# Kernel optimization log

Measured on AMD Instinct MI355X. Metric: run time of the kernel, lower is better.

Reference implementation:

```python
import jax, jax.numpy as jnp
import numpy as np

N_NODES = 30000
N_EDGES = 480000
IN_CH, NF, OUT_CH = 64, 128, 3
N_HIDDEN = 6  # GCN(num_layers=7): conv0 (in->nf) + 6 convs (nf->nf)
SLOPE = 0.02


def setup_inputs() -> dict:
    key = jax.random.key(0)
    ks = jax.random.split(key, 8)
    x = jax.random.normal(ks[0], (N_NODES, IN_CH), dtype=jnp.float32)
    edge_index = jax.random.randint(ks[1], (2, N_EDGES), 0, N_NODES, dtype=jnp.int64)
    W0 = jax.random.normal(ks[2], (IN_CH, NF), dtype=jnp.float32) * (1.0 / np.sqrt(IN_CH))
    b0 = jnp.zeros((NF,), dtype=jnp.float32)
    Wh = jax.random.normal(ks[3], (N_HIDDEN, NF, NF), dtype=jnp.float32) * (1.0 / np.sqrt(NF))
    bh = jnp.zeros((N_HIDDEN, NF), dtype=jnp.float32)
    Wout = jax.random.normal(ks[4], (NF, OUT_CH), dtype=jnp.float32) * (1.0 / np.sqrt(NF))
    bout = jnp.zeros((OUT_CH,), dtype=jnp.float32)
    return {"x": x, "edge_index": edge_index, "W0": W0, "b0": b0,
            "Wh": Wh, "bh": bh, "Wout": Wout, "bout": bout}


def _gcn_norm(edge_index, n):
    # PyG GCNConv default: add self-loops, symmetric normalization D^-1/2 (A+I) D^-1/2
    loop = jnp.arange(n, dtype=edge_index.dtype)
    src = jnp.concatenate([edge_index[0], loop])
    dst = jnp.concatenate([edge_index[1], loop])
    deg = jax.ops.segment_sum(jnp.ones_like(dst, dtype=jnp.float32), dst, num_segments=n)
    dinv = jax.lax.rsqrt(deg)  # deg >= 1 due to self-loops
    norm = dinv[src] * dinv[dst]  # [E+N]
    return src, dst, norm


def _gcn_conv(h, W, b, src, dst, norm, n):
    h = h @ W                                   # [N, F_out]
    msg = h[src] * norm[:, None]                # gather + scale  [E+N, F_out]
    out = jax.ops.segment_sum(msg, dst, num_segments=n)  # scatter-add
    return out + b


def reference(x, edge_index, W0, b0, Wh, bh, Wout, bout):
    n = x.shape[0]
    src, dst, norm = _gcn_norm(edge_index, n)
    # 7-layer GCN stack with LeakyReLU(0.02) between layers; dropout is
    # identity in eval mode (training=False).
    h = _gcn_conv(x, W0, b0, src, dst, norm, n)
    for i in range(N_HIDDEN):
        h = jax.nn.leaky_relu(h, SLOPE)
        h = _gcn_conv(h, Wh[i], bh[i], src, dst, norm, n)
    # outer forward: leaky_relu -> dropout(eval=identity) -> out conv -> tanh*0.5
    h = jax.nn.leaky_relu(h, SLOPE)
    h = _gcn_conv(h, Wout, bout, src, dst, norm, n)
    return jnp.tanh(h) * 0.5
```

## Files before the change

kernel.cpp:

```cpp
#include <hip/hip_runtime.h>
#include <hip/hip_fp16.h>
#include <math.h>

#define NN 30000
#define NE 480000
#define NB 118
#define INVSCALE (1.0f / 4096.0f)

typedef _Float16 half8 __attribute__((ext_vector_type(8)));
typedef float floatx4 __attribute__((ext_vector_type(4)));
typedef float floatx2 __attribute__((ext_vector_type(2)));

__device__ __forceinline__ float lrelu(float v) { return v > 0.0f ? v : v * 0.02f; }

__device__ __forceinline__ float4 fma4(float4 v, float w, float4 a) {
    a.x = fmaf(v.x, w, a.x);
    a.y = fmaf(v.y, w, a.y);
    a.z = fmaf(v.z, w, a.z);
    a.w = fmaf(v.w, w, a.w);
    return a;
}

__device__ __forceinline__ float4 loadh4(const __half* p) {
    uint2 raw = *(const uint2*)p;
    float2 f0 = __half22float2(*(__half2*)&raw.x);
    float2 f1 = __half22float2(*(__half2*)&raw.y);
    return make_float4(f0.x, f0.y, f1.x, f1.y);
}

__device__ __forceinline__ void loadf8x8(const unsigned char* p, float4* lo, float4* hi) {
    uint2 raw = *(const uint2*)p;
    floatx2 a = __builtin_amdgcn_cvt_pk_f32_fp8(raw.x, false);
    floatx2 b = __builtin_amdgcn_cvt_pk_f32_fp8(raw.x, true);
    floatx2 c = __builtin_amdgcn_cvt_pk_f32_fp8(raw.y, false);
    floatx2 d = __builtin_amdgcn_cvt_pk_f32_fp8(raw.y, true);
    *lo = make_float4(a.x, a.y, b.x, b.y);
    *hi = make_float4(c.x, c.y, d.x, d.y);
}

__device__ __forceinline__ void stnt_f8(unsigned char* p, float v) {
    int pk = __builtin_amdgcn_cvt_pk_fp8_f32(v, v, 0, false);
    __builtin_nontemporal_store((unsigned char)pk, p);
}


__global__ void k_count(const int* __restrict__ ei, int* __restrict__ cnt,
                        const float* __restrict__ W0, const float* __restrict__ Wh,
                        const float* __restrict__ b0, const float* __restrict__ bh,
                        const float* __restrict__ x,
                        __half* __restrict__ W0t, __half* __restrict__ Wht,
                        float* __restrict__ bs, __half* __restrict__ x16) {
    int g = blockIdx.x * 256 + threadIdx.x;
    if (g < NE) atomicAdd(&cnt[ei[NE + g]], 1);
    {
        float4 v = *(const float4*)&x[(size_t)g * 4];
        __half2 a = __floats2half2_rn(v.x, v.y);
        __half2 b = __floats2half2_rn(v.z, v.w);
        uint2 pk;
        pk.x = *(unsigned int*)&a;
        pk.y = *(unsigned int*)&b;
        *(uint2*)&x16[(size_t)g * 4] = pk;
    }
    if (g < 8192) {
        int k = g >> 7, n = g & 127;
        W0t[n * 64 + k] = __float2half(W0[g] * 64.0f);
    } else if (g < 8192 + 98304) {
        int j = g - 8192;
        int l = j >> 14;
        int r = j & 16383;
        int k = r >> 7, n = r & 127;
        Wht[l * 16384 + n * 128 + k] = __float2half(Wh[j] * 2.0f);
    } else if (g < 8192 + 98304 + 896) {
        int j = g - 8192 - 98304;
        float sc;
        if (j < 128) sc = 64.0f;
        else sc = (float)(1 << (7 + ((j - 128) >> 7)));
        bs[j] = (j < 128 ? b0[j] : bh[j - 128]) * sc;
    }
}

__global__ void k_scan1(const int* __restrict__ cnt, int* __restrict__ bsum,
                        float* __restrict__ dinv) {
    __shared__ int sd[256];
    int tid = threadIdx.x;
    int i = blockIdx.x * 256 + tid;
    int v = (i < NN) ? cnt[i] : 0;
    if (i < NN) dinv[i] = 1.0f / sqrtf((float)(v + 1));
    sd[tid] = v;
    __syncthreads();
    for (int off = 128; off > 0; off >>= 1) {
        if (tid < off) sd[tid] += sd[tid + off];
        __syncthreads();
    }
    if (tid == 0) bsum[blockIdx.x] = sd[0];
}

__global__ void k_scan3(const int* __restrict__ cnt, const int* __restrict__ bsum,
                        int* __restrict__ row_ptr, int* __restrict__ cursor) {
    __shared__ int sd[256];
    __shared__ int offs[128];
    int tid = threadIdx.x;
    if (tid < 128) offs[tid] = (tid < blockIdx.x) ? bsum[tid] : 0;
    __syncthreads();
    for (int o = 64; o > 0; o >>= 1) {
        if (tid < o) offs[tid] += offs[tid + o];
        __syncthreads();
    }
    int i = blockIdx.x * 256 + tid;
    int v = (i < NN) ? cnt[i] : 0;
    sd[tid] = v;
    __syncthreads();
    for (int off = 1; off < 256; off <<= 1) {
        int t = (tid >= off) ? sd[tid - off] : 0;
        __syncthreads();
        sd[tid] += t;
        __syncthreads();
    }
    if (i < NN) {
        int excl = offs[0] + sd[tid] - v;
        row_ptr[i] = excl;
        cursor[i] = excl;
        if (i == NN - 1) row_ptr[NN] = excl + v;
    }
}

__global__ void k_fill(const int* __restrict__ ei, const float* __restrict__ dinv,
                       int* __restrict__ cursor, int2* __restrict__ csr) {
    int e = blockIdx.x * 256 + threadIdx.x;
    if (e < NE) {
        int s = ei[e];
        int d = ei[NE + e];
        int pos = atomicAdd(&cursor[d], 1);
        float w = dinv[s] * dinv[d];
        csr[pos] = make_int2(s, __float_as_int(w));
    }
}


__launch_bounds__(256)
__global__ void k_layer0(const __half* __restrict__ x, const int* __restrict__ row_ptr,
                         const int2* __restrict__ csr, const float* __restrict__ dinv,
                         const __half* __restrict__ Wt, const float* __restrict__ bias,
                         unsigned char* __restrict__ out8) {
    __shared__ _Float16 hsF[2 * 4 * 16 * 8];
    int tid = threadIdx.x;
    int node0 = blockIdx.x * 16;
    {
        int nl = tid >> 4;
        int node = node0 + nl;
        int c = (tid & 15) * 4;
        float di = dinv[node];
        float w0 = di * di;
        float4 hv = loadh4(&x[(size_t)node * 64 + c]);
        float4 acc[8];
        acc[0] = make_float4(hv.x * w0, hv.y * w0, hv.z * w0, hv.w * w0);
        #pragma unroll
        for (int j = 1; j < 8; j++) acc[j] = make_float4(0.f, 0.f, 0.f, 0.f);
        int e = row_ptr[node];
        int e1 = row_ptr[node + 1];
        for (; e + 8 <= e1; e += 8) {
            int2 sw[8];
            #pragma unroll
            for (int j = 0; j < 8; j++) sw[j] = csr[e + j];
            float4 v[8];
            #pragma unroll
            for (int j = 0; j < 8; j++) v[j] = loadh4(&x[(size_t)sw[j].x * 64 + c]);
            #pragma unroll
            for (int j = 0; j < 8; j++) acc[j] = fma4(v[j], __int_as_float(sw[j].y), acc[j]);
        }
        for (; e < e1; ++e) {
            int2 sw = csr[e];
            float4 v = loadh4(&x[(size_t)sw.x * 64 + c]);
            acc[0] = fma4(v, __int_as_float(sw.y), acc[0]);
        }
        #pragma unroll
        for (int j = 1; j < 8; j++) {
            acc[0].x += acc[j].x;
            acc[0].y += acc[j].y;
            acc[0].z += acc[j].z;
            acc[0].w += acc[j].w;
        }
        int ks = c >> 5, quad = (c >> 3) & 3, jj = c & 7;
        __half2 p0 = __floats2half2_rn(acc[0].x, acc[0].y);
        __half2 p1 = __floats2half2_rn(acc[0].z, acc[0].w);
        uint2 pk;
        pk.x = *(unsigned int*)&p0;
        pk.y = *(unsigned int*)&p1;
        *(uint2*)&hsF[((ks * 4 + quad) * 16 + nl) * 8 + jj] = pk;
    }
    __syncthreads();
    int wave = tid >> 6, lane = tid & 63, quad = lane >> 4, ln = lane & 15;
    half8 afrag[2];
    #pragma unroll
    for (int ks = 0; ks < 2; ks++)
        afrag[ks] = *(const half8*)&hsF[((ks * 4 + quad) * 16 + ln) * 8];
    #pragma unroll
    for (int tc = 0; tc < 2; tc++) {
        int tt = wave + tc * 4;
        floatx4 acc = (floatx4){0.f, 0.f, 0.f, 0.f};
        #pragma unroll
        for (int ks = 0; ks < 2; ks++) {
            half8 b = *(const half8*)&Wt[(size_t)(tt * 16 + ln) * 64 + ks * 32 + quad * 8];
            acc = __builtin_amdgcn_mfma_f32_16x16x32_f16(afrag[ks], b, acc, 0, 0, 0);
        }
        int col = tt * 16 + ln;
        float bb = bias[col];
        #pragma unroll
        for (int r = 0; r < 4; r++) {
            int row = node0 + quad * 4 + r;
            stnt_f8(&out8[(size_t)row * 128 + col], lrelu(acc[r] + bb));
        }
    }
}

template <bool LAST>
__launch_bounds__(256)
__global__ void k_layer_h(const unsigned char* __restrict__ h, const int* __restrict__ row_ptr,
                          const int2* __restrict__ csr, const float* __restrict__ dinv,
                          const __half* __restrict__ Wt, const float* __restrict__ bias,
                          unsigned char* __restrict__ out8, const float* __restrict__ Wout,
                          float* __restrict__ u) {
    __shared__ _Float16 hsF[4 * 4 * 16 * 8];
    __shared__ float uacc[4][16][3];
    int tid = threadIdx.x;
    int node0 = blockIdx.x * 16;
    {
        int nl = tid >> 4;
        int node = node0 + nl;
        int c = (tid & 15) * 8;
        float di = dinv[node];
        float w0 = di * di;
        float4 hlo, hhi;
        loadf8x8(&h[(size_t)node * 128 + c], &hlo, &hhi);
        float4 acc[4][2];
        acc[0][0] = make_float4(hlo.x * w0, hlo.y * w0, hlo.z * w0, hlo.w * w0);
        acc[0][1] = make_float4(hhi.x * w0, hhi.y * w0, hhi.z * w0, hhi.w * w0);
        #pragma unroll
        for (int j = 1; j < 4; j++) {
            acc[j][0] = make_float4(0.f, 0.f, 0.f, 0.f);
            acc[j][1] = make_float4(0.f, 0.f, 0.f, 0.f);
        }
        int e = row_ptr[node];
        int e1 = row_ptr[node + 1];
        for (; e + 4 <= e1; e += 4) {
            int2 sw[4];
            #pragma unroll
            for (int j = 0; j < 4; j++) sw[j] = csr[e + j];
            float4 vlo[4], vhi[4];
            #pragma unroll
            for (int j = 0; j < 4; j++)
                loadf8x8(&h[(size_t)sw[j].x * 128 + c], &vlo[j], &vhi[j]);
            #pragma unroll
            for (int j = 0; j < 4; j++) {
                float w = __int_as_float(sw[j].y);
                acc[j][0] = fma4(vlo[j], w, acc[j][0]);
                acc[j][1] = fma4(vhi[j], w, acc[j][1]);
            }
        }
        for (; e < e1; ++e) {
            int2 sw = csr[e];
            float4 vlo, vhi;
            loadf8x8(&h[(size_t)sw.x * 128 + c], &vlo, &vhi);
            float w = __int_as_float(sw.y);
            acc[0][0] = fma4(vlo, w, acc[0][0]);
            acc[0][1] = fma4(vhi, w, acc[0][1]);
        }
        #pragma unroll
        for (int j = 1; j < 4; j++) {
            acc[0][0].x += acc[j][0].x; acc[0][0].y += acc[j][0].y;
            acc[0][0].z += acc[j][0].z; acc[0][0].w += acc[j][0].w;
            acc[0][1].x += acc[j][1].x; acc[0][1].y += acc[j][1].y;
            acc[0][1].z += acc[j][1].z; acc[0][1].w += acc[j][1].w;
        }
        int ks = c >> 5, quad = (c >> 3) & 3;
        __half2 p0 = __floats2half2_rn(acc[0][0].x, acc[0][0].y);
        __half2 p1 = __floats2half2_rn(acc[0][0].z, acc[0][0].w);
        __half2 p2 = __floats2half2_rn(acc[0][1].x, acc[0][1].y);
        __half2 p3 = __floats2half2_rn(acc[0][1].z, acc[0][1].w);
        uint4 pk;
        pk.x = *(unsigned int*)&p0;
        pk.y = *(unsigned int*)&p1;
        pk.z = *(unsigned int*)&p2;
        pk.w = *(unsigned int*)&p3;
        *(uint4*)&hsF[((ks * 4 + quad) * 16 + nl) * 8] = pk;
    }
    __syncthreads();
    int wave = tid >> 6, lane = tid & 63, quad = lane >> 4, ln = lane & 15;
    half8 afrag[4];
    #pragma unroll
    for (int ks = 0; ks < 4; ks++)
        afrag[ks] = *(const half8*)&hsF[((ks * 4 + quad) * 16 + ln) * 8];

    float up[4][3];
    if (LAST) {
        #pragma unroll
        for (int r = 0; r < 4; r++)
            #pragma unroll
            for (int cc = 0; cc < 3; cc++) up[r][cc] = 0.f;
    }

    #pragma unroll
    for (int tc = 0; tc < 2; tc++) {
        int tt = wave + tc * 4;
        floatx4 acc = (floatx4){0.f, 0.f, 0.f, 0.f};
        #pragma unroll
        for (int ks = 0; ks < 4; ks++) {
            half8 b = *(const half8*)&Wt[(size_t)(tt * 16 + ln) * 128 + ks * 32 + quad * 8];
            acc = __builtin_amdgcn_mfma_f32_16x16x32_f16(afrag[ks], b, acc, 0, 0, 0);
        }
        int col = tt * 16 + ln;
        float bb = bias[col];
        if (LAST) {
            float w0o = Wout[col * 3 + 0];
            float w1o = Wout[col * 3 + 1];
            float w2o = Wout[col * 3 + 2];
            #pragma unroll
            for (int r = 0; r < 4; r++) {
                float hv = lrelu(acc[r] + bb);
                up[r][0] = fmaf(hv, w0o, up[r][0]);
                up[r][1] = fmaf(hv, w1o, up[r][1]);
                up[r][2] = fmaf(hv, w2o, up[r][2]);
            }
        } else {
            #pragma unroll
            for (int r = 0; r < 4; r++) {
                int row = node0 + quad * 4 + r;
                stnt_f8(&out8[(size_t)row * 128 + col], lrelu(acc[r] + bb));
            }
        }
    }

    if (LAST) {
        #pragma unroll
        for (int m = 1; m < 16; m <<= 1) {
            #pragma unroll
            for (int r = 0; r < 4; r++) {
                #pragma unroll
                for (int cc = 0; cc < 3; cc++)
                    up[r][cc] += __shfl_xor(up[r][cc], m);
            }
        }
        if (ln == 0) {
            #pragma unroll
            for (int r = 0; r < 4; r++) {
                #pragma unroll
                for (int cc = 0; cc < 3; cc++)
                    uacc[wave][quad * 4 + r][cc] = up[r][cc];
            }
        }
        __syncthreads();
        if (tid < 48) {
            int row = tid / 3, cc = tid % 3;
            float s = (uacc[0][row][cc] + uacc[1][row][cc]) +
                      (uacc[2][row][cc] + uacc[3][row][cc]);
            u[(size_t)(node0 + row) * 3 + cc] = s;
        }
    }
}


__global__ void k_agg_out(const float* __restrict__ u, const int* __restrict__ row_ptr,
                          const int2* __restrict__ csr, const float* __restrict__ dinv,
                          const float* __restrict__ bout, float* __restrict__ out) {
    int node = blockIdx.x * 256 + threadIdx.x;
    if (node >= NN) return;
    float di = dinv[node], w0 = di * di;
    float s0 = u[(size_t)node * 3 + 0] * w0;
    float s1 = u[(size_t)node * 3 + 1] * w0;
    float s2 = u[(size_t)node * 3 + 2] * w0;
    float b0a = 0.f, b1a = 0.f, b2a = 0.f;
    int e = row_ptr[node];
    int e1 = row_ptr[node + 1];
    for (; e + 2 <= e1; e += 2) {
        int2 swa = csr[e], swb = csr[e + 1];
        float wa = __int_as_float(swa.y), wb = __int_as_float(swb.y);
        const float* ua = &u[(size_t)swa.x * 3];
        const float* ub = &u[(size_t)swb.x * 3];
        s0 = fmaf(ua[0], wa, s0);
        s1 = fmaf(ua[1], wa, s1);
        s2 = fmaf(ua[2], wa, s2);
        b0a = fmaf(ub[0], wb, b0a);
        b1a = fmaf(ub[1], wb, b1a);
        b2a = fmaf(ub[2], wb, b2a);
    }
    for (; e < e1; ++e) {
        int2 sw = csr[e];
        float w = __int_as_float(sw.y);
        const float* us = &u[(size_t)sw.x * 3];
        s0 = fmaf(us[0], w, s0);
        s1 = fmaf(us[1], w, s1);
        s2 = fmaf(us[2], w, s2);
    }
    out[(size_t)node * 3 + 0] = tanhf((s0 + b0a) * INVSCALE + bout[0]) * 0.5f;
    out[(size_t)node * 3 + 1] = tanhf((s1 + b1a) * INVSCALE + bout[1]) * 0.5f;
    out[(size_t)node * 3 + 2] = tanhf((s2 + b2a) * INVSCALE + bout[2]) * 0.5f;
}


extern "C" void kernel_launch(void* const* d_in, const int* in_sizes, int n_in,
                              void* d_out, int out_size, void* d_ws, size_t ws_size,
                              hipStream_t stream) {
    const float* x        = (const float*)d_in[0];
    const int*   ei       = (const int*)d_in[1];
    const float* W0       = (const float*)d_in[2];
    const float* b0       = (const float*)d_in[3];
    const float* Wh       = (const float*)d_in[4];
    const float* bh       = (const float*)d_in[5];
    const float* Wout     = (const float*)d_in[6];
    const float* bout     = (const float*)d_in[7];
    float* out            = (float*)d_out;

    char* ws = (char*)d_ws;
    float*  bufA   = (float*)(ws + 0);
    unsigned char* bufB8 = (unsigned char*)(ws + 15360000);
    unsigned char* bufC8 = (unsigned char*)(ws + 23040000);
    __half* x16    = (__half*)(ws + 30720000);
    __half* W0t16  = (__half*)(ws + 34560000);
    __half* Wht16  = (__half*)(ws + 34576384);
    float*  bs     = (float*)(ws + 34772992);
    float*  dinv   = (float*)(ws + 34776576);
    int*    cnt    = (int*)  (ws + 34896576);
    int*    row_ptr= (int*)  (ws + 35016576);
    int*    cursor = (int*)  (ws + 35136640);
    int2*   csr    = (int2*) (ws + 35256640);

    int* bsum = (int*)bufA;

    hipMemsetAsync(cnt, 0, NN * sizeof(int), stream);
    k_count<<<(NE + 255) / 256, 256, 0, stream>>>(ei, cnt, W0, Wh, b0, bh, x,
                                                  W0t16, Wht16, bs, x16);
    k_scan1<<<NB, 256, 0, stream>>>(cnt, bsum, dinv);
    k_scan3<<<NB, 256, 0, stream>>>(cnt, bsum, row_ptr, cursor);
    k_fill<<<(NE + 255) / 256, 256, 0, stream>>>(ei, dinv, cursor, csr);

    k_layer0<<<NN / 16, 256, 0, stream>>>(x16, row_ptr, csr, dinv, W0t16, bs, bufB8);

    unsigned char* hin = bufB8;
    unsigned char* hout = bufC8;
    for (int i = 0; i < 5; i++) {
        k_layer_h<false><<<NN / 16, 256, 0, stream>>>(hin, row_ptr, csr, dinv,
                                                      Wht16 + (size_t)i * 16384,
                                                      bs + 128 + (size_t)i * 128, hout,
                                                      Wout, bufA);
        unsigned char* t = hin; hin = hout; hout = t;
    }
    k_layer_h<true><<<NN / 16, 256, 0, stream>>>(hin, row_ptr, csr, dinv,
                                                 Wht16 + (size_t)5 * 16384,
                                                 bs + 128 + (size_t)5 * 128, hout,
                                                 Wout, bufA );

    k_agg_out<<<(NN + 255) / 256, 256, 0, stream>>>(bufA, row_ptr, csr, dinv, bout, out);
}
```

Measured before the change: 297.5 us.

## Split each node's edge gather across two half-waves and merge scans into one kernel

Layer kernels now use 512 threads per 16-node tile. Each node's neighbor list is split between two 16-lane groups that each handle 8 edges per iteration, with clamped tail loads and a shuffle reduction at the end. The MFMA stage then uses 8 waves, one output column tile each, instead of 4 waves doing two tiles each. This aims to raise memory-level parallelism for the irregular gathers, but adds predicated loads, a cross-lane reduction and more registers per block. The two-kernel prefix scan is replaced by a single 1024-thread block scan, which saves a launch but serializes the work onto one CU.

```diff
diff --git a/kernel.cpp b/kernel.cpp
--- a/kernel.cpp
+++ b/kernel.cpp
@@ -4,8 +4,9 @@
 
 #define NN 30000
 #define NE 480000
-#define NB 118
+#define NTILE 1875
 #define INVSCALE (1.0f / 4096.0f)
+
 
 typedef _Float16 half8 __attribute__((ext_vector_type(8)));
 typedef float floatx4 __attribute__((ext_vector_type(4)));
@@ -21,15 +22,13 @@
     return a;
 }
 
-__device__ __forceinline__ float4 loadh4(const __half* p) {
-    uint2 raw = *(const uint2*)p;
+__device__ __forceinline__ float4 cvth4(uint2 raw) {
     float2 f0 = __half22float2(*(__half2*)&raw.x);
     float2 f1 = __half22float2(*(__half2*)&raw.y);
     return make_float4(f0.x, f0.y, f1.x, f1.y);
 }
 
-__device__ __forceinline__ void loadf8x8(const unsigned char* p, float4* lo, float4* hi) {
-    uint2 raw = *(const uint2*)p;
+__device__ __forceinline__ void cvtf8x8(uint2 raw, float4* lo, float4* hi) {
     floatx2 a = __builtin_amdgcn_cvt_pk_f32_fp8(raw.x, false);
     floatx2 b = __builtin_amdgcn_cvt_pk_f32_fp8(raw.x, true);
     floatx2 c = __builtin_amdgcn_cvt_pk_f32_fp8(raw.y, false);
@@ -41,6 +40,14 @@
 __device__ __forceinline__ void stnt_f8(unsigned char* p, float v) {
     int pk = __builtin_amdgcn_cvt_pk_fp8_f32(v, v, 0, false);
     __builtin_nontemporal_store((unsigned char)pk, p);
+}
+
+__device__ __forceinline__ float4 xadd16(float4 a) {
+    a.x += __shfl_xor(a.x, 16);
+    a.y += __shfl_xor(a.y, 16);
+    a.z += __shfl_xor(a.z, 16);
+    a.w += __shfl_xor(a.w, 16);
+    return a;
 }
 
 
@@ -79,49 +86,52 @@
     }
 }
 
-__global__ void k_scan1(const int* __restrict__ cnt, int* __restrict__ bsum,
-                        float* __restrict__ dinv) {
-    __shared__ int sd[256];
+__global__ void k_scan(const int* __restrict__ cnt, int* __restrict__ row_ptr,
+                       int* __restrict__ cursor, float* __restrict__ dinv) {
+    __shared__ int part[1024];
     int tid = threadIdx.x;
-    int i = blockIdx.x * 256 + tid;
-    int v = (i < NN) ? cnt[i] : 0;
-    if (i < NN) dinv[i] = 1.0f / sqrtf((float)(v + 1));
-    sd[tid] = v;
+    const int CH = 32;
+    int base = tid * CH;
+    int s = 0;
+    #pragma unroll
+    for (int i = 0; i < CH; i += 4) {
+        int idx = base + i;
+        if (idx < NN) {
+            int4 v = *(const int4*)&cnt[idx];
+            s += v.x + v.y + v.z + v.w;
+        }
+    }
+    part[tid] = s;
     __syncthreads();
-    for (int off = 128; off > 0; off >>= 1) {
-        if (tid < off) sd[tid] += sd[tid + off];
+    for (int off = 1; off < 1024; off <<= 1) {
+        int t = (tid >= off) ? part[tid - off] : 0;
         __syncthreads();
-    }
-    if (tid == 0) bsum[blockIdx.x] = sd[0];
-}
-
-__global__ void k_scan3(const int* __restrict__ cnt, const int* __restrict__ bsum,
-                        int* __restrict__ row_ptr, int* __restrict__ cursor) {
-    __shared__ int sd[256];
-    __shared__ int offs[128];
-    int tid = threadIdx.x;
-    if (tid < 128) offs[tid] = (tid < blockIdx.x) ? bsum[tid] : 0;
-    __syncthreads();
-    for (int o = 64; o > 0; o >>= 1) {
-        if (tid < o) offs[tid] += offs[tid + o];
+        part[tid] += t;
         __syncthreads();
     }
-    int i = blockIdx.x * 256 + tid;
-    int v = (i < NN) ? cnt[i] : 0;
-    sd[tid] = v;
-    __syncthreads();
-    for (int off = 1; off < 256; off <<= 1) {
-        int t = (tid >= off) ? sd[tid - off] : 0;
-        __syncthreads();
-        sd[tid] += t;
-        __syncthreads();
-    }
-    if (i < NN) {
-        int excl = offs[0] + sd[tid] - v;
-        row_ptr[i] = excl;
-        cursor[i] = excl;
-        if (i == NN - 1) row_ptr[NN] = excl + v;
-    }
+    int run = part[tid] - s;
+    #pragma unroll
+    for (int i = 0; i < CH; i += 4) {
+        int idx = base + i;
+        if (idx < NN) {
+            int4 v = *(const int4*)&cnt[idx];
+            int4 rp;
+            rp.x = run;
+            rp.y = rp.x + v.x;
+            rp.z = rp.y + v.y;
+            rp.w = rp.z + v.z;
+            run = rp.w + v.w;
+            *(int4*)&row_ptr[idx] = rp;
+            *(int4*)&cursor[idx] = rp;
+            float4 dv;
+            dv.x = 1.0f / sqrtf((float)(v.x + 1));
+            dv.y = 1.0f / sqrtf((float)(v.y + 1));
+            dv.z = 1.0f / sqrtf((float)(v.z + 1));
+            dv.w = 1.0f / sqrtf((float)(v.w + 1));
+            *(float4*)&dinv[idx] = dv;
+        }
+    }
+    if (tid == 1023) row_ptr[NN] = part[1023];
 }
 
 __global__ void k_fill(const int* __restrict__ ei, const float* __restrict__ dinv,
@@ -137,7 +147,7 @@
 }
 
 
-__launch_bounds__(256)
+__launch_bounds__(512)
 __global__ void k_layer0(const __half* __restrict__ x, const int* __restrict__ row_ptr,
                          const int2* __restrict__ csr, const float* __restrict__ dinv,
                          const __half* __restrict__ Wt, const float* __restrict__ bias,
@@ -146,191 +156,173 @@
     int tid = threadIdx.x;
     int node0 = blockIdx.x * 16;
     {
-        int nl = tid >> 4;
+        int nl = tid >> 5;
+        int sub = (tid >> 4) & 1;
+        int c = (tid & 15) * 4;
         int node = node0 + nl;
-        int c = (tid & 15) * 4;
-        float di = dinv[node];
-        float w0 = di * di;
-        float4 hv = loadh4(&x[(size_t)node * 64 + c]);
-        float4 acc[8];
-        acc[0] = make_float4(hv.x * w0, hv.y * w0, hv.z * w0, hv.w * w0);
+        float4 acc[4];
         #pragma unroll
-        for (int j = 1; j < 8; j++) acc[j] = make_float4(0.f, 0.f, 0.f, 0.f);
-        int e = row_ptr[node];
+        for (int j = 0; j < 4; j++) acc[j] = make_float4(0.f, 0.f, 0.f, 0.f);
+        if (sub == 0) {
+            float di = dinv[node];
+            float w0 = di * di;
+            float4 hv = cvth4(*(const uint2*)&x[(size_t)node * 64 + c]);
+            acc[0] = make_float4(hv.x * w0, hv.y * w0, hv.z * w0, hv.w * w0);
+        }
+        int e0 = row_ptr[node];
         int e1 = row_ptr[node + 1];
-        for (; e + 8 <= e1; e += 8) {
+        for (int ee = e0 + sub * 8; ee < e1; ee += 16) {
             int2 sw[8];
-            #pragma unroll
-            for (int j = 0; j < 8; j++) sw[j] = csr[e + j];
-            float4 v[8];
-            #pragma unroll
-            for (int j = 0; j < 8; j++) v[j] = loadh4(&x[(size_t)sw[j].x * 64 + c]);
-            #pragma unroll
-            for (int j = 0; j < 8; j++) acc[j] = fma4(v[j], __int_as_float(sw[j].y), acc[j]);
-        }
-        for (; e < e1; ++e) {
-            int2 sw = csr[e];
-            float4 v = loadh4(&x[(size_t)sw.x * 64 + c]);
-            acc[0] = fma4(v, __int_as_float(sw.y), acc[0]);
-        }
-        #pragma unroll
-        for (int j = 1; j < 8; j++) {
-            acc[0].x += acc[j].x;
-            acc[0].y += acc[j].y;
-            acc[0].z += acc[j].z;
-            acc[0].w += acc[j].w;
-        }
-        int ks = c >> 5, quad = (c >> 3) & 3, jj = c & 7;
-        __half2 p0 = __floats2half2_rn(acc[0].x, acc[0].y);
-        __half2 p1 = __floats2half2_rn(acc[0].z, acc[0].w);
-        uint2 pk;
-        pk.x = *(unsigned int*)&p0;
-        pk.y = *(unsigned int*)&p1;
-        *(uint2*)&hsF[((ks * 4 + quad) * 16 + nl) * 8 + jj] = pk;
+            uint2 raw[8];
+            #pragma unroll
+            for (int j = 0; j < 8; j++) {
+                int idx = (ee + j < e1) ? ee + j : e1 - 1;
+                sw[j] = csr[idx];
+            }
+            #pragma unroll
+            for (int j = 0; j < 8; j++)
+                raw[j] = *(const uint2*)&x[(size_t)sw[j].x * 64 + c];
+            #pragma unroll
+            for (int j = 0; j < 8; j++) {
+                float w = (ee + j < e1) ? __int_as_float(sw[j].y) : 0.f;
+                acc[j & 3] = fma4(cvth4(raw[j]), w, acc[j & 3]);
+            }
+        }
+        acc[0].x += acc[1].x + acc[2].x + acc[3].x;
+        acc[0].y += acc[1].y + acc[2].y + acc[3].y;
+        acc[0].z += acc[1].z + acc[2].z + acc[3].z;
+        acc[0].w += acc[1].w + acc[2].w + acc[3].w;
+        acc[0] = xadd16(acc[0]);
+        if (sub == 0) {
+            int ks = c >> 5, quad = (c >> 3) & 3, jj = c & 7;
+            __half2 p0 = __floats2half2_rn(acc[0].x, acc[0].y);
+            __half2 p1 = __floats2half2_rn(acc[0].z, acc[0].w);
+            uint2 pk;
+            pk.x = *(unsigned int*)&p0;
+            pk.y = *(unsigned int*)&p1;
+            *(uint2*)&hsF[((ks * 4 + quad) * 16 + nl) * 8 + jj] = pk;
+        }
     }
     __syncthreads();
-    int wave = tid >> 6, lane = tid & 63, quad = lane >> 4, ln = lane & 15;
+    int tt = tid >> 6, lane = tid & 63, quad = lane >> 4, ln = lane & 15;
     half8 afrag[2];
     #pragma unroll
     for (int ks = 0; ks < 2; ks++)
         afrag[ks] = *(const half8*)&hsF[((ks * 4 + quad) * 16 + ln) * 8];
-    #pragma unroll
-    for (int tc = 0; tc < 2; tc++) {
-        int tt = wave + tc * 4;
-        floatx4 acc = (floatx4){0.f, 0.f, 0.f, 0.f};
-        #pragma unroll
-        for (int ks = 0; ks < 2; ks++) {
-            half8 b = *(const half8*)&Wt[(size_t)(tt * 16 + ln) * 64 + ks * 32 + quad * 8];
-            acc = __builtin_amdgcn_mfma_f32_16x16x32_f16(afrag[ks], b, acc, 0, 0, 0);
-        }
-        int col = tt * 16 + ln;
-        float bb = bias[col];
-        #pragma unroll
-        for (int r = 0; r < 4; r++) {
-            int row = node0 + quad * 4 + r;
-            stnt_f8(&out8[(size_t)row * 128 + col], lrelu(acc[r] + bb));
-        }
+    floatx4 acc = (floatx4){0.f, 0.f, 0.f, 0.f};
+    #pragma unroll
+    for (int ks = 0; ks < 2; ks++) {
+        half8 b = *(const half8*)&Wt[(size_t)(tt * 16 + ln) * 64 + ks * 32 + quad * 8];
+        acc = __builtin_amdgcn_mfma_f32_16x16x32_f16(afrag[ks], b, acc, 0, 0, 0);
+    }
+    int col = tt * 16 + ln;
+    float bb = bias[col];
+    #pragma unroll
+    for (int r = 0; r < 4; r++) {
+        int row = node0 + quad * 4 + r;
+        stnt_f8(&out8[(size_t)row * 128 + col], lrelu(acc[r] + bb));
     }
 }
 
 template <bool LAST>
-__launch_bounds__(256)
+__launch_bounds__(512)
 __global__ void k_layer_h(const unsigned char* __restrict__ h, const int* __restrict__ row_ptr,
                           const int2* __restrict__ csr, const float* __restrict__ dinv,
                           const __half* __restrict__ Wt, const float* __restrict__ bias,
                           unsigned char* __restrict__ out8, const float* __restrict__ Wout,
                           float* __restrict__ u) {
     __shared__ _Float16 hsF[4 * 4 * 16 * 8];
-    __shared__ float uacc[4][16][3];
+    __shared__ float uaccS[8][16][3];
     int tid = threadIdx.x;
     int node0 = blockIdx.x * 16;
     {
-        int nl = tid >> 4;
+        int nl = tid >> 5;
+        int sub = (tid >> 4) & 1;
+        int c = (tid & 15) * 8;
         int node = node0 + nl;
-        int c = (tid & 15) * 8;
-        float di = dinv[node];
-        float w0 = di * di;
-        float4 hlo, hhi;
-        loadf8x8(&h[(size_t)node * 128 + c], &hlo, &hhi);
-        float4 acc[4][2];
-        acc[0][0] = make_float4(hlo.x * w0, hlo.y * w0, hlo.z * w0, hlo.w * w0);
-        acc[0][1] = make_float4(hhi.x * w0, hhi.y * w0, hhi.z * w0, hhi.w * w0);
+        float4 acc[2][2];
         #pragma unroll
-        for (int j = 1; j < 4; j++) {
+        for (int j = 0; j < 2; j++) {
             acc[j][0] = make_float4(0.f, 0.f, 0.f, 0.f);
             acc[j][1] = make_float4(0.f, 0.f, 0.f, 0.f);
         }
-        int e = row_ptr[node];
+        if (sub == 0) {
+            float di = dinv[node];
+            float w0 = di * di;
+            float4 hlo, hhi;
+            cvtf8x8(*(const uint2*)&h[(size_t)node * 128 + c], &hlo, &hhi);
+            acc[0][0] = make_float4(hlo.x * w0, hlo.y * w0, hlo.z * w0, hlo.w * w0);
+            acc[0][1] = make_float4(hhi.x * w0, hhi.y * w0, hhi.z * w0, hhi.w * w0);
+        }
+        int e0 = row_ptr[node];
         int e1 = row_ptr[node + 1];
-        for (; e + 4 <= e1; e += 4) {
-            int2 sw[4];
-            #pragma unroll
-            for (int j = 0; j < 4; j++) sw[j] = csr[e + j];
-            float4 vlo[4], vhi[4];
-            #pragma unroll
-            for (int j = 0; j < 4; j++)
-                loadf8x8(&h[(size_t)sw[j].x * 128 + c], &vlo[j], &vhi[j]);
-            #pragma unroll
-            for (int j = 0; j < 4; j++) {
-                float w = __int_as_float(sw[j].y);
-                acc[j][0] = fma4(vlo[j], w, acc[j][0]);
-                acc[j][1] = fma4(vhi[j], w, acc[j][1]);
-            }
-        }
-        for (; e < e1; ++e) {
-            int2 sw = csr[e];
-            float4 vlo, vhi;
-            loadf8x8(&h[(size_t)sw.x * 128 + c], &vlo, &vhi);
-            float w = __int_as_float(sw.y);
-            acc[0][0] = fma4(vlo, w, acc[0][0]);
-            acc[0][1] = fma4(vhi, w, acc[0][1]);
-        }
-        #pragma unroll
-        for (int j = 1; j < 4; j++) {
-            acc[0][0].x += acc[j][0].x; acc[0][0].y += acc[j][0].y;
-            acc[0][0].z += acc[j][0].z; acc[0][0].w += acc[j][0].w;
-            acc[0][1].x += acc[j][1].x; acc[0][1].y += acc[j][1].y;
-            acc[0][1].z += acc[j][1].z; acc[0][1].w += acc[j][1].w;
-        }
-        int ks = c >> 5, quad = (c >> 3) & 3;
-        __half2 p0 = __floats2half2_rn(acc[0][0].x, acc[0][0].y);
-        __half2 p1 = __floats2half2_rn(acc[0][0].z, acc[0][0].w);
-        __half2 p2 = __floats2half2_rn(acc[0][1].x, acc[0][1].y);
-        __half2 p3 = __floats2half2_rn(acc[0][1].z, acc[0][1].w);
-        uint4 pk;
-        pk.x = *(unsigned int*)&p0;
-        pk.y = *(unsigned int*)&p1;
-        pk.z = *(unsigned int*)&p2;
-        pk.w = *(unsigned int*)&p3;
-        *(uint4*)&hsF[((ks * 4 + quad) * 16 + nl) * 8] = pk;
+        for (int ee = e0 + sub * 8; ee < e1; ee += 16) {
+            int2 sw[8];
+            uint2 raw[8];
+            #pragma unroll
+            for (int j = 0; j < 8; j++) {
+                int idx = (ee + j < e1) ? ee + j : e1 - 1;
+                sw[j] = csr[idx];
+            }
+            #pragma unroll
+            for (int j = 0; j < 8; j++)
+                raw[j] = *(const uint2*)&h[(size_t)sw[j].x * 128 + c];
+            #pragma unroll
+            for (int j = 0; j < 8; j++) {
+                float w = (ee + j < e1) ? __int_as_float(sw[j].y) : 0.f;
+                float4 vlo, vhi;
+                cvtf8x8(raw[j], &vlo, &vhi);
+                acc[j & 1][0] = fma4(vlo, w, acc[j & 1][0]);
+                acc[j & 1][1] = fma4(vhi, w, acc[j & 1][1]);
+            }
+        }
+        acc[0][0].x += acc[1][0].x; acc[0][0].y += acc[1][0].y;
+        acc[0][0].z += acc[1][0].z; acc[0][0].w += acc[1][0].w;
+        acc[0][1].x += acc[1][1].x; acc[0][1].y += acc[1][1].y;
+        acc[0][1].z += acc[1][1].z; acc[0][1].w += acc[1][1].w;
+        acc[0][0] = xadd16(acc[0][0]);
+        acc[0][1] = xadd16(acc[0][1]);
+        if (sub == 0) {
+            int ks = c >> 5, quad = (c >> 3) & 3;
+            __half2 p0 = __floats2half2_rn(acc[0][0].x, acc[0][0].y);
+            __half2 p1 = __floats2half2_rn(acc[0][0].z, acc[0][0].w);
+            __half2 p2 = __floats2half2_rn(acc[0][1].x, acc[0][1].y);
+            __half2 p3 = __floats2half2_rn(acc[0][1].z, acc[0][1].w);
+            uint4 pk;
+            pk.x = *(unsigned int*)&p0;
+            pk.y = *(unsigned int*)&p1;
+            pk.z = *(unsigned int*)&p2;
+            pk.w = *(unsigned int*)&p3;
+            *(uint4*)&hsF[((ks * 4 + quad) * 16 + nl) * 8] = pk;
+        }
     }
     __syncthreads();
-    int wave = tid >> 6, lane = tid & 63, quad = lane >> 4, ln = lane & 15;
+    int tt = tid >> 6, lane = tid & 63, quad = lane >> 4, ln = lane & 15;
     half8 afrag[4];
     #pragma unroll
     for (int ks = 0; ks < 4; ks++)
         afrag[ks] = *(const half8*)&hsF[((ks * 4 + quad) * 16 + ln) * 8];
 
-    float up[4][3];
+    floatx4 acc = (floatx4){0.f, 0.f, 0.f, 0.f};
+    #pragma unroll
+    for (int ks = 0; ks < 4; ks++) {
+        half8 b = *(const half8*)&Wt[(size_t)(tt * 16 + ln) * 128 + ks * 32 + quad * 8];
+        acc = __builtin_amdgcn_mfma_f32_16x16x32_f16(afrag[ks], b, acc, 0, 0, 0);
+    }
+    int col = tt * 16 + ln;
+    float bb = bias[col];
     if (LAST) {
+        float up[4][3];
+        float w0o = Wout[col * 3 + 0];
+        float w1o = Wout[col * 3 + 1];
+        float w2o = Wout[col * 3 + 2];
         #pragma unroll
-        for (int r = 0; r < 4; r++)
-            #pragma unroll
-            for (int cc = 0; cc < 3; cc++) up[r][cc] = 0.f;
-    }
-
-    #pragma unroll
-    for (int tc = 0; tc < 2; tc++) {
-        int tt = wave + tc * 4;
-        floatx4 acc = (floatx4){0.f, 0.f, 0.f, 0.f};
-        #pragma unroll
-        for (int ks = 0; ks < 4; ks++) {
-            half8 b = *(const half8*)&Wt[(size_t)(tt * 16 + ln) * 128 + ks * 32 + quad * 8];
-            acc = __builtin_amdgcn_mfma_f32_16x16x32_f16(afrag[ks], b, acc, 0, 0, 0);
-        }
-        int col = tt * 16 + ln;
-        float bb = bias[col];
-        if (LAST) {
-            float w0o = Wout[col * 3 + 0];
-            float w1o = Wout[col * 3 + 1];
-            float w2o = Wout[col * 3 + 2];
-            #pragma unroll
-            for (int r = 0; r < 4; r++) {
-                float hv = lrelu(acc[r] + bb);
-                up[r][0] = fmaf(hv, w0o, up[r][0]);
-                up[r][1] = fmaf(hv, w1o, up[r][1]);
-                up[r][2] = fmaf(hv, w2o, up[r][2]);
-            }
-        } else {
-            #pragma unroll
-            for (int r = 0; r < 4; r++) {
-                int row = node0 + quad * 4 + r;
-                stnt_f8(&out8[(size_t)row * 128 + col], lrelu(acc[r] + bb));
-            }
-        }
-    }
-
-    if (LAST) {
+        for (int r = 0; r < 4; r++) {
+            float hv = lrelu(acc[r] + bb);
+            up[r][0] = hv * w0o;
+            up[r][1] = hv * w1o;
+            up[r][2] = hv * w2o;
+        }
         #pragma unroll
         for (int m = 1; m < 16; m <<= 1) {
             #pragma unroll
@@ -345,15 +337,22 @@
             for (int r = 0; r < 4; r++) {
                 #pragma unroll
                 for (int cc = 0; cc < 3; cc++)
-                    uacc[wave][quad * 4 + r][cc] = up[r][cc];
+                    uaccS[tt][quad * 4 + r][cc] = up[r][cc];
             }
         }
         __syncthreads();
         if (tid < 48) {
             int row = tid / 3, cc = tid % 3;
-            float s = (uacc[0][row][cc] + uacc[1][row][cc]) +
-                      (uacc[2][row][cc] + uacc[3][row][cc]);
+            float s = 0.f;
+            #pragma unroll
+            for (int t = 0; t < 8; t++) s += uaccS[t][row][cc];
             u[(size_t)(node0 + row) * 3 + cc] = s;
+        }
+    } else {
+        #pragma unroll
+        for (int r = 0; r < 4; r++) {
+            int row = node0 + quad * 4 + r;
+            stnt_f8(&out8[(size_t)row * 128 + col], lrelu(acc[r] + bb));
         }
     }
 }
@@ -424,30 +423,27 @@
     int*    cursor = (int*)  (ws + 35136640);
     int2*   csr    = (int2*) (ws + 35256640);
 
-    int* bsum = (int*)bufA;
-
     hipMemsetAsync(cnt, 0, NN * sizeof(int), stream);
     k_count<<<(NE + 255) / 256, 256, 0, stream>>>(ei, cnt, W0, Wh, b0, bh, x,
                                                   W0t16, Wht16, bs, x16);
-    k_scan1<<<NB, 256, 0, stream>>>(cnt, bsum, dinv);
-    k_scan3<<<NB, 256, 0, stream>>>(cnt, bsum, row_ptr, cursor);
+    k_scan<<<1, 1024, 0, stream>>>(cnt, row_ptr, cursor, dinv);
     k_fill<<<(NE + 255) / 256, 256, 0, stream>>>(ei, dinv, cursor, csr);
 
-    k_layer0<<<NN / 16, 256, 0, stream>>>(x16, row_ptr, csr, dinv, W0t16, bs, bufB8);
+    k_layer0<<<NTILE, 512, 0, stream>>>(x16, row_ptr, csr, dinv, W0t16, bs, bufB8);
 
     unsigned char* hin = bufB8;
     unsigned char* hout = bufC8;
     for (int i = 0; i < 5; i++) {
-        k_layer_h<false><<<NN / 16, 256, 0, stream>>>(hin, row_ptr, csr, dinv,
-                                                      Wht16 + (size_t)i * 16384,
-                                                      bs + 128 + (size_t)i * 128, hout,
-                                                      Wout, bufA);
+        k_layer_h<false><<<NTILE, 512, 0, stream>>>(hin, row_ptr, csr, dinv,
+                                                    Wht16 + (size_t)i * 16384,
+                                                    bs + 128 + (size_t)i * 128, hout,
+                                                    Wout, bufA);
         unsigned char* t = hin; hin = hout; hout = t;
     }
-    k_layer_h<true><<<NN / 16, 256, 0, stream>>>(hin, row_ptr, csr, dinv,
-                                                 Wht16 + (size_t)5 * 16384,
-                                                 bs + 128 + (size_t)5 * 128, hout,
-                                                 Wout, bufA );
+    k_layer_h<true><<<NTILE, 512, 0, stream>>>(hin, row_ptr, csr, dinv,
+                                               Wht16 + (size_t)5 * 16384,
+                                               bs + 128 + (size_t)5 * 128, hout,
+                                               Wout, bufA );
 
     k_agg_out<<<(NN + 255) / 256, 256, 0, stream>>>(bufA, row_ptr, csr, dinv, bout, out);
 }
```

After: 324.0 us. 8.9% more time.

## Deepen gather batches with predication, prefetch feature lines, switch to cached stores

Applied to the files above, without the earlier changes.

The neighbor-gather loops in the layer kernels now issue 16 predicated edge loads per batch, with out-of-range weights zeroed and no scalar tail loop, using two accumulators instead of four or eight. Each block also loads one word per 64-byte line of a chunk of the input feature matrix to warm the cache, and an empty asm statement keeps those loads from being removed. Output stores switch from nontemporal to normal so that the next layer's gathers can hit in cache, and a waves_per_eu hint is added. The goal is more memory-level parallelism and better cache reuse, at the cost of higher register pressure, extra prefetch traffic and wasted loads on short rows.

```diff
diff --git a/kernel.cpp b/kernel.cpp
--- a/kernel.cpp
+++ b/kernel.cpp
@@ -5,7 +5,9 @@
 #define NN 30000
 #define NE 480000
 #define NB 118
+#define NTILE 1875
 #define INVSCALE (1.0f / 4096.0f)
+
 
 typedef _Float16 half8 __attribute__((ext_vector_type(8)));
 typedef float floatx4 __attribute__((ext_vector_type(4)));
@@ -21,15 +23,13 @@
     return a;
 }
 
-__device__ __forceinline__ float4 loadh4(const __half* p) {
-    uint2 raw = *(const uint2*)p;
+__device__ __forceinline__ float4 cvth4(uint2 raw) {
     float2 f0 = __half22float2(*(__half2*)&raw.x);
     float2 f1 = __half22float2(*(__half2*)&raw.y);
     return make_float4(f0.x, f0.y, f1.x, f1.y);
 }
 
-__device__ __forceinline__ void loadf8x8(const unsigned char* p, float4* lo, float4* hi) {
-    uint2 raw = *(const uint2*)p;
+__device__ __forceinline__ void cvtf8x8(uint2 raw, float4* lo, float4* hi) {
     floatx2 a = __builtin_amdgcn_cvt_pk_f32_fp8(raw.x, false);
     floatx2 b = __builtin_amdgcn_cvt_pk_f32_fp8(raw.x, true);
     floatx2 c = __builtin_amdgcn_cvt_pk_f32_fp8(raw.y, false);
@@ -38,9 +38,19 @@
     *hi = make_float4(c.x, c.y, d.x, d.y);
 }
 
-__device__ __forceinline__ void stnt_f8(unsigned char* p, float v) {
+__device__ __forceinline__ void loadf8x8(const unsigned char* p, float4* lo, float4* hi) {
+    cvtf8x8(*(const uint2*)p, lo, hi);
+}
+
+__device__ __forceinline__ void st_f8(unsigned char* p, float v) {
     int pk = __builtin_amdgcn_cvt_pk_fp8_f32(v, v, 0, false);
-    __builtin_nontemporal_store((unsigned char)pk, p);
+    *p = (unsigned char)pk;
+}
+
+__device__ __forceinline__ unsigned int pf_line(const void* base, int bid, int tid) {
+    size_t off = ((size_t)(bid >> 3) * 256 + (size_t)tid) * 64;
+    if (off < (size_t)NN * 128) return *(const unsigned int*)((const char*)base + off);
+    return 0u;
 }
 
 
@@ -138,6 +148,7 @@
 
 
 __launch_bounds__(256)
+__attribute__((amdgpu_waves_per_eu(4)))
 __global__ void k_layer0(const __half* __restrict__ x, const int* __restrict__ row_ptr,
                          const int2* __restrict__ csr, const float* __restrict__ dinv,
                          const __half* __restrict__ Wt, const float* __restrict__ bias,
@@ -145,41 +156,39 @@
     __shared__ _Float16 hsF[2 * 4 * 16 * 8];
     int tid = threadIdx.x;
     int node0 = blockIdx.x * 16;
+    unsigned int pf = pf_line(x, blockIdx.x, tid);
     {
         int nl = tid >> 4;
         int node = node0 + nl;
         int c = (tid & 15) * 4;
         float di = dinv[node];
         float w0 = di * di;
-        float4 hv = loadh4(&x[(size_t)node * 64 + c]);
-        float4 acc[8];
+        float4 hv = cvth4(*(const uint2*)&x[(size_t)node * 64 + c]);
+        float4 acc[2];
         acc[0] = make_float4(hv.x * w0, hv.y * w0, hv.z * w0, hv.w * w0);
-        #pragma unroll
-        for (int j = 1; j < 8; j++) acc[j] = make_float4(0.f, 0.f, 0.f, 0.f);
-        int e = row_ptr[node];
-        int e1 = row_ptr[node + 1];
-        for (; e + 8 <= e1; e += 8) {
-            int2 sw[8];
-            #pragma unroll
-            for (int j = 0; j < 8; j++) sw[j] = csr[e + j];
-            float4 v[8];
-            #pragma unroll
-            for (int j = 0; j < 8; j++) v[j] = loadh4(&x[(size_t)sw[j].x * 64 + c]);
-            #pragma unroll
-            for (int j = 0; j < 8; j++) acc[j] = fma4(v[j], __int_as_float(sw[j].y), acc[j]);
-        }
-        for (; e < e1; ++e) {
-            int2 sw = csr[e];
-            float4 v = loadh4(&x[(size_t)sw.x * 64 + c]);
-            acc[0] = fma4(v, __int_as_float(sw.y), acc[0]);
-        }
-        #pragma unroll
-        for (int j = 1; j < 8; j++) {
-            acc[0].x += acc[j].x;
-            acc[0].y += acc[j].y;
-            acc[0].z += acc[j].z;
-            acc[0].w += acc[j].w;
-        }
+        acc[1] = make_float4(0.f, 0.f, 0.f, 0.f);
+        int e0r = row_ptr[node];
+        int e1r = row_ptr[node + 1];
+        for (int ee = e0r; ee < e1r; ee += 16) {
+            int2 sw[16];
+            #pragma unroll
+            for (int j = 0; j < 16; j++)
+                sw[j] = csr[(ee + j < e1r) ? ee + j : e1r - 1];
+            uint2 raw[16];
+            float wv[16];
+            #pragma unroll
+            for (int j = 0; j < 16; j++) {
+                raw[j] = *(const uint2*)&x[(size_t)sw[j].x * 64 + c];
+                wv[j] = (ee + j < e1r) ? __int_as_float(sw[j].y) : 0.f;
+            }
+            #pragma unroll
+            for (int j = 0; j < 16; j++)
+                acc[j & 1] = fma4(cvth4(raw[j]), wv[j], acc[j & 1]);
+        }
+        acc[0].x += acc[1].x;
+        acc[0].y += acc[1].y;
+        acc[0].z += acc[1].z;
+        acc[0].w += acc[1].w;
         int ks = c >> 5, quad = (c >> 3) & 3, jj = c & 7;
         __half2 p0 = __floats2half2_rn(acc[0].x, acc[0].y);
         __half2 p1 = __floats2half2_rn(acc[0].z, acc[0].w);
@@ -188,6 +197,7 @@
         pk.y = *(unsigned int*)&p1;
         *(uint2*)&hsF[((ks * 4 + quad) * 16 + nl) * 8 + jj] = pk;
     }
+    asm volatile("" :: "v"(pf));
     __syncthreads();
     int wave = tid >> 6, lane = tid & 63, quad = lane >> 4, ln = lane & 15;
     half8 afrag[2];
@@ -208,13 +218,14 @@
         #pragma unroll
         for (int r = 0; r < 4; r++) {
             int row = node0 + quad * 4 + r;
-            stnt_f8(&out8[(size_t)row * 128 + col], lrelu(acc[r] + bb));
+            st_f8(&out8[(size_t)row * 128 + col], lrelu(acc[r] + bb));
         }
     }
 }
 
 template <bool LAST>
 __launch_bounds__(256)
+__attribute__((amdgpu_waves_per_eu(4)))
 __global__ void k_layer_h(const unsigned char* __restrict__ h, const int* __restrict__ row_ptr,
                           const int2* __restrict__ csr, const float* __restrict__ dinv,
                           const __half* __restrict__ Wt, const float* __restrict__ bias,
@@ -224,6 +235,7 @@
     __shared__ float uacc[4][16][3];
     int tid = threadIdx.x;
     int node0 = blockIdx.x * 16;
+    unsigned int pf = pf_line(h, blockIdx.x, tid);
     {
         int nl = tid >> 4;
         int node = node0 + nl;
@@ -232,46 +244,37 @@
         float w0 = di * di;
         float4 hlo, hhi;
         loadf8x8(&h[(size_t)node * 128 + c], &hlo, &hhi);
-        float4 acc[4][2];
+        float4 acc[2][2];
         acc[0][0] = make_float4(hlo.x * w0, hlo.y * w0, hlo.z * w0, hlo.w * w0);
         acc[0][1] = make_float4(hhi.x * w0, hhi.y * w0, hhi.z * w0, hhi.w * w0);
-        #pragma unroll
-        for (int j = 1; j < 4; j++) {
-            acc[j][0] = make_float4(0.f, 0.f, 0.f, 0.f);
-            acc[j][1] = make_float4(0.f, 0.f, 0.f, 0.f);
-        }
-        int e = row_ptr[node];
-        int e1 = row_ptr[node + 1];
-        for (; e + 4 <= e1; e += 4) {
-            int2 sw[4];
-            #pragma unroll
-            for (int j = 0; j < 4; j++) sw[j] = csr[e + j];
-            float4 vlo[4], vhi[4];
-            #pragma unroll
-            for (int j = 0; j < 4; j++)
-                loadf8x8(&h[(size_t)sw[j].x * 128 + c], &vlo[j], &vhi[j]);
-            #pragma unroll
-            for (int j = 0; j < 4; j++) {
-                float w = __int_as_float(sw[j].y);
-                acc[j][0] = fma4(vlo[j], w, acc[j][0]);
-                acc[j][1] = fma4(vhi[j], w, acc[j][1]);
-            }
-        }
-        for (; e < e1; ++e) {
-            int2 sw = csr[e];
-            float4 vlo, vhi;
-            loadf8x8(&h[(size_t)sw.x * 128 + c], &vlo, &vhi);
-            float w = __int_as_float(sw.y);
-            acc[0][0] = fma4(vlo, w, acc[0][0]);
-            acc[0][1] = fma4(vhi, w, acc[0][1]);
-        }
-        #pragma unroll
-        for (int j = 1; j < 4; j++) {
-            acc[0][0].x += acc[j][0].x; acc[0][0].y += acc[j][0].y;
-            acc[0][0].z += acc[j][0].z; acc[0][0].w += acc[j][0].w;
-            acc[0][1].x += acc[j][1].x; acc[0][1].y += acc[j][1].y;
-            acc[0][1].z += acc[j][1].z; acc[0][1].w += acc[j][1].w;
-        }
+        acc[1][0] = make_float4(0.f, 0.f, 0.f, 0.f);
+        acc[1][1] = make_float4(0.f, 0.f, 0.f, 0.f);
+        int e0r = row_ptr[node];
+        int e1r = row_ptr[node + 1];
+        for (int ee = e0r; ee < e1r; ee += 16) {
+            int2 sw[16];
+            #pragma unroll
+            for (int j = 0; j < 16; j++)
+                sw[j] = csr[(ee + j < e1r) ? ee + j : e1r - 1];
+            uint2 raw[16];
+            float wv[16];
+            #pragma unroll
+            for (int j = 0; j < 16; j++) {
+                raw[j] = *(const uint2*)&h[(size_t)sw[j].x * 128 + c];
+                wv[j] = (ee + j < e1r) ? __int_as_float(sw[j].y) : 0.f;
+            }
+            #pragma unroll
+            for (int j = 0; j < 16; j++) {
+                float4 vlo, vhi;
+                cvtf8x8(raw[j], &vlo, &vhi);
+                acc[j & 1][0] = fma4(vlo, wv[j], acc[j & 1][0]);
+                acc[j & 1][1] = fma4(vhi, wv[j], acc[j & 1][1]);
+            }
+        }
+        acc[0][0].x += acc[1][0].x; acc[0][0].y += acc[1][0].y;
+        acc[0][0].z += acc[1][0].z; acc[0][0].w += acc[1][0].w;
+        acc[0][1].x += acc[1][1].x; acc[0][1].y += acc[1][1].y;
+        acc[0][1].z += acc[1][1].z; acc[0][1].w += acc[1][1].w;
         int ks = c >> 5, quad = (c >> 3) & 3;
         __half2 p0 = __floats2half2_rn(acc[0][0].x, acc[0][0].y);
         __half2 p1 = __floats2half2_rn(acc[0][0].z, acc[0][0].w);
@@ -284,6 +287,7 @@
         pk.w = *(unsigned int*)&p3;
         *(uint4*)&hsF[((ks * 4 + quad) * 16 + nl) * 8] = pk;
     }
+    asm volatile("" :: "v"(pf));
     __syncthreads();
     int wave = tid >> 6, lane = tid & 63, quad = lane >> 4, ln = lane & 15;
     half8 afrag[4];
@@ -325,7 +329,7 @@
             #pragma unroll
             for (int r = 0; r < 4; r++) {
                 int row = node0 + quad * 4 + r;
-                stnt_f8(&out8[(size_t)row * 128 + col], lrelu(acc[r] + bb));
+                st_f8(&out8[(size_t)row * 128 + col], lrelu(acc[r] + bb));
             }
         }
     }
@@ -433,21 +437,21 @@
     k_scan3<<<NB, 256, 0, stream>>>(cnt, bsum, row_ptr, cursor);
     k_fill<<<(NE + 255) / 256, 256, 0, stream>>>(ei, dinv, cursor, csr);
 
-    k_layer0<<<NN / 16, 256, 0, stream>>>(x16, row_ptr, csr, dinv, W0t16, bs, bufB8);
+    k_layer0<<<NTILE, 256, 0, stream>>>(x16, row_ptr, csr, dinv, W0t16, bs, bufB8);
 
     unsigned char* hin = bufB8;
     unsigned char* hout = bufC8;
     for (int i = 0; i < 5; i++) {
-        k_layer_h<false><<<NN / 16, 256, 0, stream>>>(hin, row_ptr, csr, dinv,
-                                                      Wht16 + (size_t)i * 16384,
-                                                      bs + 128 + (size_t)i * 128, hout,
-                                                      Wout, bufA);
+        k_layer_h<false><<<NTILE, 256, 0, stream>>>(hin, row_ptr, csr, dinv,
+                                                    Wht16 + (size_t)i * 16384,
+                                                    bs + 128 + (size_t)i * 128, hout,
+                                                    Wout, bufA);
         unsigned char* t = hin; hin = hout; hout = t;
     }
-    k_layer_h<true><<<NN / 16, 256, 0, stream>>>(hin, row_ptr, csr, dinv,
-                                                 Wht16 + (size_t)5 * 16384,
-                                                 bs + 128 + (size_t)5 * 128, hout,
-                                                 Wout, bufA );
+    k_layer_h<true><<<NTILE, 256, 0, stream>>>(hin, row_ptr, csr, dinv,
+                                               Wht16 + (size_t)5 * 16384,
+                                               bs + 128 + (size_t)5 * 128, hout,
+                                               Wout, bufA );
 
     k_agg_out<<<(NN + 255) / 256, 256, 0, stream>>>(bufA, row_ptr, csr, dinv, bout, out);
 }
```

Result: slower. 324.8 us (+9.2%).

## Balance edge aggregation across block threads with shared-memory atomic accumulation

Applied to the files above, without the earlier changes.

Hidden layers no longer give each 16-thread group one destination node's edge list. The block's whole contiguous CSR edge range is split into 8-edge chunks spread over all thread groups. Partial sums are flushed into a shared float accumulator with LDS atomics whenever the destination changes. The destination's low 4 bits are packed into the low mantissa bits of the edge weight so the owning node can be recovered without another load. This evens out load imbalance from skewed degrees and raises memory-level parallelism, at the cost of LDS atomics, extra syncs, more shared memory and a slightly perturbed weight.

```diff
diff --git a/kernel.cpp b/kernel.cpp
--- a/kernel.cpp
+++ b/kernel.cpp
@@ -6,6 +6,7 @@
 #define NE 480000
 #define NB 118
 #define INVSCALE (1.0f / 4096.0f)
+
 
 typedef _Float16 half8 __attribute__((ext_vector_type(8)));
 typedef float floatx4 __attribute__((ext_vector_type(4)));
@@ -28,14 +29,17 @@
     return make_float4(f0.x, f0.y, f1.x, f1.y);
 }
 
-__device__ __forceinline__ void loadf8x8(const unsigned char* p, float4* lo, float4* hi) {
-    uint2 raw = *(const uint2*)p;
+__device__ __forceinline__ void cvtf8x8(uint2 raw, float4* lo, float4* hi) {
     floatx2 a = __builtin_amdgcn_cvt_pk_f32_fp8(raw.x, false);
     floatx2 b = __builtin_amdgcn_cvt_pk_f32_fp8(raw.x, true);
     floatx2 c = __builtin_amdgcn_cvt_pk_f32_fp8(raw.y, false);
     floatx2 d = __builtin_amdgcn_cvt_pk_f32_fp8(raw.y, true);
     *lo = make_float4(a.x, a.y, b.x, b.y);
     *hi = make_float4(c.x, c.y, d.x, d.y);
+}
+
+__device__ __forceinline__ void loadf8x8(const unsigned char* p, float4* lo, float4* hi) {
+    cvtf8x8(*(const uint2*)p, lo, hi);
 }
 
 __device__ __forceinline__ void stnt_f8(unsigned char* p, float v) {
@@ -132,7 +136,8 @@
         int d = ei[NE + e];
         int pos = atomicAdd(&cursor[d], 1);
         float w = dinv[s] * dinv[d];
-        csr[pos] = make_int2(s, __float_as_int(w));
+        unsigned int wb = (__float_as_uint(w) & ~15u) | (unsigned int)(d & 15);
+        csr[pos] = make_int2(s, (int)wb);
     }
 }
 
@@ -220,71 +225,97 @@
                           const __half* __restrict__ Wt, const float* __restrict__ bias,
                           unsigned char* __restrict__ out8, const float* __restrict__ Wout,
                           float* __restrict__ u) {
+    __shared__ float accF[16][128];
     __shared__ _Float16 hsF[4 * 4 * 16 * 8];
     __shared__ float uacc[4][16][3];
     int tid = threadIdx.x;
     int node0 = blockIdx.x * 16;
+    int et = tid >> 4;
+    int c = (tid & 15) * 8;
+
     {
-        int nl = tid >> 4;
-        int node = node0 + nl;
-        int c = (tid & 15) * 8;
+        int node = node0 + et;
         float di = dinv[node];
         float w0 = di * di;
         float4 hlo, hhi;
         loadf8x8(&h[(size_t)node * 128 + c], &hlo, &hhi);
-        float4 acc[4][2];
-        acc[0][0] = make_float4(hlo.x * w0, hlo.y * w0, hlo.z * w0, hlo.w * w0);
-        acc[0][1] = make_float4(hhi.x * w0, hhi.y * w0, hhi.z * w0, hhi.w * w0);
-        #pragma unroll
-        for (int j = 1; j < 4; j++) {
-            acc[j][0] = make_float4(0.f, 0.f, 0.f, 0.f);
-            acc[j][1] = make_float4(0.f, 0.f, 0.f, 0.f);
-        }
-        int e = row_ptr[node];
-        int e1 = row_ptr[node + 1];
-        for (; e + 4 <= e1; e += 4) {
-            int2 sw[4];
-            #pragma unroll
-            for (int j = 0; j < 4; j++) sw[j] = csr[e + j];
-            float4 vlo[4], vhi[4];
-            #pragma unroll
-            for (int j = 0; j < 4; j++)
-                loadf8x8(&h[(size_t)sw[j].x * 128 + c], &vlo[j], &vhi[j]);
-            #pragma unroll
-            for (int j = 0; j < 4; j++) {
-                float w = __int_as_float(sw[j].y);
-                acc[j][0] = fma4(vlo[j], w, acc[j][0]);
-                acc[j][1] = fma4(vhi[j], w, acc[j][1]);
-            }
-        }
-        for (; e < e1; ++e) {
-            int2 sw = csr[e];
-            float4 vlo, vhi;
-            loadf8x8(&h[(size_t)sw.x * 128 + c], &vlo, &vhi);
-            float w = __int_as_float(sw.y);
-            acc[0][0] = fma4(vlo, w, acc[0][0]);
-            acc[0][1] = fma4(vhi, w, acc[0][1]);
-        }
-        #pragma unroll
-        for (int j = 1; j < 4; j++) {
-            acc[0][0].x += acc[j][0].x; acc[0][0].y += acc[j][0].y;
-            acc[0][0].z += acc[j][0].z; acc[0][0].w += acc[j][0].w;
-            acc[0][1].x += acc[j][1].x; acc[0][1].y += acc[j][1].y;
-            acc[0][1].z += acc[j][1].z; acc[0][1].w += acc[j][1].w;
-        }
+        *(float4*)&accF[et][c] = make_float4(hlo.x * w0, hlo.y * w0, hlo.z * w0, hlo.w * w0);
+        *(float4*)&accF[et][c + 4] = make_float4(hhi.x * w0, hhi.y * w0, hhi.z * w0, hhi.w * w0);
+    }
+    __syncthreads();
+
+    {
+        int e0 = row_ptr[node0];
+        int e1 = row_ptr[node0 + 16];
+        for (int base = e0 + et * 8; base < e1; base += 16 * 8) {
+            int n = e1 - base;
+            if (n > 8) n = 8;
+            int2 sw[8];
+            #pragma unroll
+            for (int j = 0; j < 8; j++) sw[j] = csr[base + ((j < n) ? j : n - 1)];
+            uint2 raw[8];
+            #pragma unroll
+            for (int j = 0; j < 8; j++) raw[j] = *(const uint2*)&h[(size_t)sw[j].x * 128 + c];
+            int cur = -1;
+            float4 a0 = make_float4(0.f, 0.f, 0.f, 0.f);
+            float4 a1 = make_float4(0.f, 0.f, 0.f, 0.f);
+            #pragma unroll
+            for (int j = 0; j < 8; j++) {
+                if (j < n) {
+                    int dl = sw[j].y & 15;
+                    if (dl != cur) {
+                        if (cur >= 0) {
+                            atomicAdd(&accF[cur][c + 0], a0.x);
+                            atomicAdd(&accF[cur][c + 1], a0.y);
+                            atomicAdd(&accF[cur][c + 2], a0.z);
+                            atomicAdd(&accF[cur][c + 3], a0.w);
+                            atomicAdd(&accF[cur][c + 4], a1.x);
+                            atomicAdd(&accF[cur][c + 5], a1.y);
+                            atomicAdd(&accF[cur][c + 6], a1.z);
+                            atomicAdd(&accF[cur][c + 7], a1.w);
+                        }
+                        cur = dl;
+                        a0 = make_float4(0.f, 0.f, 0.f, 0.f);
+                        a1 = make_float4(0.f, 0.f, 0.f, 0.f);
+                    }
+                    float4 vlo, vhi;
+                    cvtf8x8(raw[j], &vlo, &vhi);
+                    float w = __int_as_float(sw[j].y);
+                    a0 = fma4(vlo, w, a0);
+                    a1 = fma4(vhi, w, a1);
+                }
+            }
+            if (cur >= 0) {
+                atomicAdd(&accF[cur][c + 0], a0.x);
+                atomicAdd(&accF[cur][c + 1], a0.y);
+                atomicAdd(&accF[cur][c + 2], a0.z);
+                atomicAdd(&accF[cur][c + 3], a0.w);
+                atomicAdd(&accF[cur][c + 4], a1.x);
+                atomicAdd(&accF[cur][c + 5], a1.y);
+                atomicAdd(&accF[cur][c + 6], a1.z);
+                atomicAdd(&accF[cur][c + 7], a1.w);
+            }
+        }
+    }
+    __syncthreads();
+
+    {
         int ks = c >> 5, quad = (c >> 3) & 3;
-        __half2 p0 = __floats2half2_rn(acc[0][0].x, acc[0][0].y);
-        __half2 p1 = __floats2half2_rn(acc[0][0].z, acc[0][0].w);
-        __half2 p2 = __floats2half2_rn(acc[0][1].x, acc[0][1].y);
-        __half2 p3 = __floats2half2_rn(acc[0][1].z, acc[0][1].w);
+        float4 s0 = *(const float4*)&accF[et][c];
+        float4 s1 = *(const float4*)&accF[et][c + 4];
+        __half2 p0 = __floats2half2_rn(s0.x, s0.y);
+        __half2 p1 = __floats2half2_rn(s0.z, s0.w);
+        __half2 p2 = __floats2half2_rn(s1.x, s1.y);
+        __half2 p3 = __floats2half2_rn(s1.z, s1.w);
         uint4 pk;
         pk.x = *(unsigned int*)&p0;
         pk.y = *(unsigned int*)&p1;
         pk.z = *(unsigned int*)&p2;
         pk.w = *(unsigned int*)&p3;
-        *(uint4*)&hsF[((ks * 4 + quad) * 16 + nl) * 8] = pk;
-    }
-    __syncthreads();
+        *(uint4*)&hsF[((ks * 4 + quad) * 16 + et) * 8] = pk;
+    }
+    __syncthreads();
+
     int wave = tid >> 6, lane = tid & 63, quad = lane >> 4, ln = lane & 15;
     half8 afrag[4];
     #pragma unroll
```

Measured after the change: 569.6 us. 91.5% more time.
